# Performance work log

Measured on AMD Instinct MI355X. Metric: run time of the kernel, lower is better.

Reference implementation:

```python
import jax, jax.numpy as jnp
import numpy as np

QMAX = 127.0

def setup_inputs() -> dict:
    key = jax.random.key(0)
    k1, k2, k3 = jax.random.split(key, 3)
    x = jax.random.normal(k1, (4, 2048, 2048), dtype=jnp.float32)
    weight = jax.random.normal(k2, (2048, 2048), dtype=jnp.float32)  # [out, in]
    bias = jax.random.normal(k3, (2048,), dtype=jnp.float32)
    return {"x": x, "weight": weight, "bias": bias}

def _quantize(t):
    # per-tensor abs-max symmetric int8 quantization
    scale = jnp.max(jnp.abs(t)) / QMAX
    q = jnp.clip(jnp.round(t / scale), -128.0, 127.0).astype(jnp.int8)
    return q, scale

def reference(x, weight, bias):
    orig_shape = x.shape
    x2 = x.reshape(-1, x.shape[-1])                      # [tokens, in]
    x_q, in_scale = _quantize(x2)
    w_q, w_scale = _quantize(weight)                     # weight: [out, in]
    # int8 GEMM accumulated in int32: [tokens, out]
    acc = jnp.matmul(x_q.astype(jnp.int32), w_q.T.astype(jnp.int32))
    # dequant (output_scale = 1.0) + bias epilogue
    out = acc.astype(jnp.float32) * (in_scale * w_scale) + bias[None, :]
    return out.reshape(*orig_shape[:-1], weight.shape[0])
```

## Files before the change

kernel.cpp:

```cpp
#include <hip/hip_runtime.h>
#include <stdint.h>

#define GK 2048
#define GN 2048
#define GM 8192

#define NVX (GM * (unsigned)GK / 4)
#define NVW (GN * (unsigned)GK / 4)

#define XBLK 512
#define WBLK 128
#define QXBLK 4096
#define QWBLK 1024

typedef int i32x4 __attribute__((ext_vector_type(4)));

__device__ __forceinline__ float amax4(float4 v) {
    return fmaxf(fmaxf(fabsf(v.x), fabsf(v.y)), fmaxf(fabsf(v.z), fabsf(v.w)));
}

__global__ __launch_bounds__(256) void absmax_kernel(
    const float4* __restrict__ xv, const float4* __restrict__ wv,
    float* __restrict__ partial)
{
    const bool isx = blockIdx.x < XBLK;
    const float4* __restrict__ src = isx ? xv : wv;
    const unsigned n      = isx ? NVX : NVW;
    const unsigned b0     = isx ? blockIdx.x : blockIdx.x - XBLK;
    const unsigned stride = (isx ? XBLK : WBLK) * 256u;

    unsigned i = b0 * 256u + threadIdx.x;
    float m = 0.f;
    for (; i + 3u * stride < n; i += 4u * stride) {
        float4 a = src[i];
        float4 b = src[i + stride];
        float4 c = src[i + 2u * stride];
        float4 d = src[i + 3u * stride];
        m = fmaxf(m, fmaxf(fmaxf(amax4(a), amax4(b)),
                           fmaxf(amax4(c), amax4(d))));
    }
    for (; i < n; i += stride) m = fmaxf(m, amax4(src[i]));

    #pragma unroll
    for (int off = 32; off > 0; off >>= 1)
        m = fmaxf(m, __shfl_xor(m, off, 64));

    __shared__ float sm[4];
    const int wid = threadIdx.x >> 6;
    if ((threadIdx.x & 63) == 0) sm[wid] = m;
    __syncthreads();
    if (threadIdx.x == 0)
        partial[blockIdx.x] = fmaxf(fmaxf(sm[0], sm[1]), fmaxf(sm[2], sm[3]));
}

__global__ __launch_bounds__(256) void scale_kernel(
    const float* __restrict__ partial, float* __restrict__ scales)
{
    const int t = threadIdx.x;
    float mx = fmaxf(partial[t], partial[t + 256]);
    float mw = (t < WBLK) ? partial[XBLK + t] : 0.f;
    #pragma unroll
    for (int off = 32; off > 0; off >>= 1) {
        mx = fmaxf(mx, __shfl_xor(mx, off, 64));
        mw = fmaxf(mw, __shfl_xor(mw, off, 64));
    }
    __shared__ float smx[4], smw[4];
    const int wid = t >> 6;
    if ((t & 63) == 0) { smx[wid] = mx; smw[wid] = mw; }
    __syncthreads();
    if (t == 0) {
        float ax = fmaxf(fmaxf(smx[0], smx[1]), fmaxf(smx[2], smx[3]));
        float aw = fmaxf(fmaxf(smw[0], smw[1]), fmaxf(smw[2], smw[3]));
        float sx = ax / 127.0f;
        float sw = aw / 127.0f;
        scales[0] = sx;
        scales[1] = sw;
        scales[2] = sx * sw;
    }
}

__device__ __forceinline__ signed char quant1(float v, float s) {
    float r = rintf(v / s);
    r = fminf(fmaxf(r, -128.f), 127.f);
    return (signed char)(int)r;
}

__device__ __forceinline__ char4 quantv(float4 v, float s) {
    char4 q;
    q.x = quant1(v.x, s); q.y = quant1(v.y, s);
    q.z = quant1(v.z, s); q.w = quant1(v.w, s);
    return q;
}

__global__ __launch_bounds__(256) void quant_kernel(
    const float4* __restrict__ xv, const float4* __restrict__ wv,
    const float* __restrict__ scales,
    char4* __restrict__ xq, char4* __restrict__ wq)
{
    const bool isx = blockIdx.x < QXBLK;
    const float s = isx ? scales[0] : scales[1];
    const float4* __restrict__ src = isx ? xv : wv;
    char4* __restrict__ dst        = isx ? xq : wq;
    const unsigned b0     = isx ? blockIdx.x : blockIdx.x - QXBLK;
    const unsigned stride = (isx ? QXBLK : QWBLK) * 256u;
    const unsigned t      = b0 * 256u + threadIdx.x;

    float4 a = src[t];
    float4 b = src[t + stride];
    float4 c = src[t + 2u * stride];
    float4 d = src[t + 3u * stride];
    dst[t]               = quantv(a, s);
    dst[t + stride]      = quantv(b, s);
    dst[t + 2u * stride] = quantv(c, s);
    dst[t + 3u * stride] = quantv(d, s);
}

__global__ __launch_bounds__(256) void gemm_kernel(
    const signed char* __restrict__ Aq,
    const signed char* __restrict__ Bq,
    const float* __restrict__ bias,
    const float* __restrict__ scales,
    float* __restrict__ out)
{
    __shared__ signed char sA[128 * 128];
    __shared__ signed char sB[128 * 128];

    const int tid  = threadIdx.x;
    const int lane = tid & 63;
    const int wid  = tid >> 6;
    const int wr   = wid >> 1;
    const int wc   = wid & 1;
    const int bn   = blockIdx.x & 15;
    const int bm   = blockIdx.x >> 4;

    const int srow  = tid >> 3;
    const int sslot = tid & 7;

    i32x4 acc[4][4] = {};

    const long Abase = (long)bm * 128 * GK;
    const long Bbase = (long)bn * 128 * GK;

    for (int kt = 0; kt < GK; kt += 128) {
        #pragma unroll
        for (int j = 0; j < 4; ++j) {
            const int row  = j * 32 + srow;
            const int slot = sslot ^ (row & 7);
            const signed char* src = Aq + Abase + (long)row * GK + kt + slot * 16;
            __builtin_amdgcn_global_load_lds(
                (const __attribute__((address_space(1))) void*)src,
                (__attribute__((address_space(3))) void*)(sA + j * 4096 + wid * 1024),
                16, 0, 0);
        }
        #pragma unroll
        for (int j = 0; j < 4; ++j) {
            const int row  = j * 32 + srow;
            const int slot = sslot ^ (row & 7);
            const signed char* src = Bq + Bbase + (long)row * GK + kt + slot * 16;
            __builtin_amdgcn_global_load_lds(
                (const __attribute__((address_space(1))) void*)src,
                (__attribute__((address_space(3))) void*)(sB + j * 4096 + wid * 1024),
                16, 0, 0);
        }
        __syncthreads();

        #pragma unroll
        for (int kk = 0; kk < 2; ++kk) {
            i32x4 af[4], bf[4];
            const int g = kk * 4 + (lane >> 4);
            #pragma unroll
            for (int m = 0; m < 4; ++m) {
                const int row = wr * 64 + m * 16 + (lane & 15);
                af[m] = *(const i32x4*)(sA + row * 128 + ((g ^ (row & 7)) << 4));
            }
            #pragma unroll
            for (int n = 0; n < 4; ++n) {
                const int row = wc * 64 + n * 16 + (lane & 15);
                bf[n] = *(const i32x4*)(sB + row * 128 + ((g ^ (row & 7)) << 4));
            }
            #pragma unroll
            for (int m = 0; m < 4; ++m)
                #pragma unroll
                for (int n = 0; n < 4; ++n)
                    acc[m][n] = __builtin_amdgcn_mfma_i32_16x16x64_i8(
                        af[m], bf[n], acc[m][n], 0, 0, 0);
        }
        __syncthreads();
    }

    const float s = scales[2];
    const int orow0 = bm * 128 + wr * 64 + (lane >> 4) * 4;
    const int ocol0 = bn * 128 + wc * 64 + (lane & 15);
    #pragma unroll
    for (int n = 0; n < 4; ++n) {
        const int col = ocol0 + n * 16;
        const float bv = bias[col];
        #pragma unroll
        for (int m = 0; m < 4; ++m) {
            const int row = orow0 + m * 16;
            #pragma unroll
            for (int i = 0; i < 4; ++i) {
                out[(long)(row + i) * GN + col] = (float)acc[m][n][i] * s + bv;
            }
        }
    }
}

extern "C" void kernel_launch(void* const* d_in, const int* in_sizes, int n_in,
                              void* d_out, int out_size, void* d_ws, size_t ws_size,
                              hipStream_t stream) {
    const float* x    = (const float*)d_in[0];
    const float* w    = (const float*)d_in[1];
    const float* bias = (const float*)d_in[2];
    float* out = (float*)d_out;

    const size_t need = 4096 + (size_t)GM * GK + (size_t)GN * GK;
    if (ws_size < need) return;

    float* scales    = (float*)d_ws;
    float* partial   = (float*)d_ws + 4;
    signed char* xq  = (signed char*)d_ws + 4096;
    signed char* wq  = xq + (size_t)GM * GK;

    absmax_kernel<<<XBLK + WBLK, 256, 0, stream>>>(
        (const float4*)x, (const float4*)w, partial);
    scale_kernel<<<1, 256, 0, stream>>>(partial, scales);
    quant_kernel<<<QXBLK + QWBLK, 256, 0, stream>>>(
        (const float4*)x, (const float4*)w, scales, (char4*)xq, (char4*)wq);
    gemm_kernel<<<(GM / 128) * (GN / 128), 256, 0, stream>>>(
        xq, wq, bias, scales, out);
}
```

Baseline: 181.0 us.

## Use 32x32x32 int8 MFMA, swizzle block order, double absmax blocks

Replaces the 16x16x64 int8 MFMA tiles in the GEMM with 32x32x32 int8 MFMAs (2x2 per wave), which cuts LDS fragment loads per MFMA. It also remaps workgroup IDs so consecutive blocks are spread across the 8 XCDs, aiming at better L2 reuse of A/B tiles. The absmax reduction launches twice as many blocks for more parallelism, so the partial-buffer workspace offset grows. The epilogue is rewritten to match the 32x32 accumulator layout, with a risk of higher register pressure.

```diff
diff --git a/kernel.cpp b/kernel.cpp
--- a/kernel.cpp
+++ b/kernel.cpp
@@ -8,12 +8,13 @@
 #define NVX (GM * (unsigned)GK / 4)
 #define NVW (GN * (unsigned)GK / 4)
 
-#define XBLK 512
-#define WBLK 128
+#define XBLK 1024
+#define WBLK 256
 #define QXBLK 4096
 #define QWBLK 1024
 
-typedef int i32x4 __attribute__((ext_vector_type(4)));
+typedef int i32x4  __attribute__((ext_vector_type(4)));
+typedef int i32x16 __attribute__((ext_vector_type(16)));
 
 __device__ __forceinline__ float amax4(float4 v) {
     return fmaxf(fmaxf(fabsf(v.x), fabsf(v.y)), fmaxf(fabsf(v.z), fabsf(v.w)));
@@ -57,8 +58,9 @@
     const float* __restrict__ partial, float* __restrict__ scales)
 {
     const int t = threadIdx.x;
-    float mx = fmaxf(partial[t], partial[t + 256]);
-    float mw = (t < WBLK) ? partial[XBLK + t] : 0.f;
+    float mx = fmaxf(fmaxf(partial[t], partial[t + 256]),
+                     fmaxf(partial[t + 512], partial[t + 768]));
+    float mw = partial[XBLK + t];
     #pragma unroll
     for (int off = 32; off > 0; off >>= 1) {
         mx = fmaxf(mx, __shfl_xor(mx, off, 64));
@@ -130,13 +132,15 @@
     const int wid  = tid >> 6;
     const int wr   = wid >> 1;
     const int wc   = wid & 1;
-    const int bn   = blockIdx.x & 15;
-    const int bm   = blockIdx.x >> 4;
+
+    const int wgid = ((blockIdx.x & 7) << 7) | (blockIdx.x >> 3);
+    const int bn   = wgid & 15;
+    const int bm   = wgid >> 4;
 
     const int srow  = tid >> 3;
     const int sslot = tid & 7;
 
-    i32x4 acc[4][4] = {};
+    i32x16 acc[2][2] = {};
 
     const long Abase = (long)bm * 128 * GK;
     const long Bbase = (long)bn * 128 * GK;
@@ -165,42 +169,42 @@
         __syncthreads();
 
         #pragma unroll
-        for (int kk = 0; kk < 2; ++kk) {
-            i32x4 af[4], bf[4];
-            const int g = kk * 4 + (lane >> 4);
-            #pragma unroll
-            for (int m = 0; m < 4; ++m) {
-                const int row = wr * 64 + m * 16 + (lane & 15);
-                af[m] = *(const i32x4*)(sA + row * 128 + ((g ^ (row & 7)) << 4));
+        for (int ks = 0; ks < 4; ++ks) {
+            const int sl = ks * 2 + (lane >> 5);
+            i32x4 af[2], bf[2];
+            #pragma unroll
+            for (int m = 0; m < 2; ++m) {
+                const int row = wr * 64 + m * 32 + (lane & 31);
+                af[m] = *(const i32x4*)(sA + row * 128 + ((sl ^ (row & 7)) << 4));
             }
             #pragma unroll
-            for (int n = 0; n < 4; ++n) {
-                const int row = wc * 64 + n * 16 + (lane & 15);
-                bf[n] = *(const i32x4*)(sB + row * 128 + ((g ^ (row & 7)) << 4));
+            for (int n = 0; n < 2; ++n) {
+                const int row = wc * 64 + n * 32 + (lane & 31);
+                bf[n] = *(const i32x4*)(sB + row * 128 + ((sl ^ (row & 7)) << 4));
             }
             #pragma unroll
-            for (int m = 0; m < 4; ++m)
+            for (int m = 0; m < 2; ++m)
                 #pragma unroll
-                for (int n = 0; n < 4; ++n)
-                    acc[m][n] = __builtin_amdgcn_mfma_i32_16x16x64_i8(
+                for (int n = 0; n < 2; ++n)
+                    acc[m][n] = __builtin_amdgcn_mfma_i32_32x32x32_i8(
                         af[m], bf[n], acc[m][n], 0, 0, 0);
         }
         __syncthreads();
     }
 
     const float s = scales[2];
-    const int orow0 = bm * 128 + wr * 64 + (lane >> 4) * 4;
-    const int ocol0 = bn * 128 + wc * 64 + (lane & 15);
+    const int orow0 = bm * 128 + wr * 64 + 4 * (lane >> 5);
+    const int ocol0 = bn * 128 + wc * 64 + (lane & 31);
     #pragma unroll
-    for (int n = 0; n < 4; ++n) {
-        const int col = ocol0 + n * 16;
+    for (int n = 0; n < 2; ++n) {
+        const int col = ocol0 + n * 32;
         const float bv = bias[col];
         #pragma unroll
-        for (int m = 0; m < 4; ++m) {
-            const int row = orow0 + m * 16;
-            #pragma unroll
-            for (int i = 0; i < 4; ++i) {
-                out[(long)(row + i) * GN + col] = (float)acc[m][n][i] * s + bv;
+        for (int m = 0; m < 2; ++m) {
+            #pragma unroll
+            for (int r = 0; r < 16; ++r) {
+                const int row = orow0 + m * 32 + (r & 3) + 8 * (r >> 2);
+                out[(long)row * GN + col] = (float)acc[m][n][r] * s + bv;
             }
         }
     }
@@ -214,12 +218,12 @@
     const float* bias = (const float*)d_in[2];
     float* out = (float*)d_out;
 
-    const size_t need = 4096 + (size_t)GM * GK + (size_t)GN * GK;
+    const size_t need = 8192 + (size_t)GM * GK + (size_t)GN * GK;
     if (ws_size < need) return;
 
     float* scales    = (float*)d_ws;
     float* partial   = (float*)d_ws + 4;
-    signed char* xq  = (signed char*)d_ws + 4096;
+    signed char* xq  = (signed char*)d_ws + 8192;
     signed char* wq  = xq + (size_t)GM * GK;
 
     absmax_kernel<<<XBLK + WBLK, 256, 0, stream>>>(
```

New measurement: 181.0 us. No clear change (+0.0%).

## Double-buffer 256x256 int8 GEMM tiles and fold scale reduction into consumers

Applied to the files above, without the earlier changes.

The GEMM now uses 256x256 output tiles with 512 threads and a double-buffered 128KB LDS. The next K-tile is prefetched with global_load_lds while MFMAs run on the current one, using s_setprio and split barriers, and block IDs are remapped for better L2 locality. The separate scale kernel is removed: every quant and GEMM block re-reduces the absmax partials itself, and the partial counts are doubled. This removes one launch and hides load latency, at the cost of heavier LDS use (one block per CU), higher register pressure, and redundant per-block reductions.

```diff
diff --git a/kernel.cpp b/kernel.cpp
--- a/kernel.cpp
+++ b/kernel.cpp
@@ -8,10 +8,11 @@
 #define NVX (GM * (unsigned)GK / 4)
 #define NVW (GN * (unsigned)GK / 4)
 
-#define XBLK 512
-#define WBLK 128
+#define XBLK 1024
+#define WBLK 256
 #define QXBLK 4096
 #define QWBLK 1024
+#define NT (GK / 128)
 
 typedef int i32x4 __attribute__((ext_vector_type(4)));
 
@@ -53,30 +54,25 @@
         partial[blockIdx.x] = fmaxf(fmaxf(sm[0], sm[1]), fmaxf(sm[2], sm[3]));
 }
 
-__global__ __launch_bounds__(256) void scale_kernel(
-    const float* __restrict__ partial, float* __restrict__ scales)
-{
-    const int t = threadIdx.x;
-    float mx = fmaxf(partial[t], partial[t + 256]);
-    float mw = (t < WBLK) ? partial[XBLK + t] : 0.f;
-    #pragma unroll
-    for (int off = 32; off > 0; off >>= 1) {
-        mx = fmaxf(mx, __shfl_xor(mx, off, 64));
-        mw = fmaxf(mw, __shfl_xor(mw, off, 64));
-    }
+__device__ __forceinline__ void reduce_scales(const float* __restrict__ partial,
+                                              int tid, float* ax_out, float* aw_out)
+{
     __shared__ float smx[4], smw[4];
-    const int wid = t >> 6;
-    if ((t & 63) == 0) { smx[wid] = mx; smw[wid] = mw; }
+    float mx = 0.f, mw = 0.f;
+    if (tid < 256) {
+        mx = fmaxf(fmaxf(partial[tid], partial[tid + 256]),
+                   fmaxf(partial[tid + 512], partial[tid + 768]));
+        mw = partial[1024 + tid];
+        #pragma unroll
+        for (int off = 32; off > 0; off >>= 1) {
+            mx = fmaxf(mx, __shfl_xor(mx, off, 64));
+            mw = fmaxf(mw, __shfl_xor(mw, off, 64));
+        }
+        if ((tid & 63) == 0) { smx[tid >> 6] = mx; smw[tid >> 6] = mw; }
+    }
     __syncthreads();
-    if (t == 0) {
-        float ax = fmaxf(fmaxf(smx[0], smx[1]), fmaxf(smx[2], smx[3]));
-        float aw = fmaxf(fmaxf(smw[0], smw[1]), fmaxf(smw[2], smw[3]));
-        float sx = ax / 127.0f;
-        float sw = aw / 127.0f;
-        scales[0] = sx;
-        scales[1] = sw;
-        scales[2] = sx * sw;
-    }
+    *ax_out = fmaxf(fmaxf(smx[0], smx[1]), fmaxf(smx[2], smx[3]));
+    *aw_out = fmaxf(fmaxf(smw[0], smw[1]), fmaxf(smw[2], smw[3]));
 }
 
 __device__ __forceinline__ signed char quant1(float v, float s) {
@@ -94,11 +90,14 @@
 
 __global__ __launch_bounds__(256) void quant_kernel(
     const float4* __restrict__ xv, const float4* __restrict__ wv,
-    const float* __restrict__ scales,
+    const float* __restrict__ partial,
     char4* __restrict__ xq, char4* __restrict__ wq)
 {
+    float ax, aw;
+    reduce_scales(partial, threadIdx.x, &ax, &aw);
+
     const bool isx = blockIdx.x < QXBLK;
-    const float s = isx ? scales[0] : scales[1];
+    const float s = (isx ? ax : aw) / 127.0f;
     const float4* __restrict__ src = isx ? xv : wv;
     char4* __restrict__ dst        = isx ? xq : wq;
     const unsigned b0     = isx ? blockIdx.x : blockIdx.x - QXBLK;
@@ -115,93 +114,130 @@
     dst[t + 3u * stride] = quantv(d, s);
 }
 
-__global__ __launch_bounds__(256) void gemm_kernel(
+__global__ __launch_bounds__(512, 2) void gemm_kernel(
     const signed char* __restrict__ Aq,
     const signed char* __restrict__ Bq,
     const float* __restrict__ bias,
-    const float* __restrict__ scales,
+    const float* __restrict__ partial,
     float* __restrict__ out)
 {
-    __shared__ signed char sA[128 * 128];
-    __shared__ signed char sB[128 * 128];
+    __shared__ signed char lds[131072];
 
     const int tid  = threadIdx.x;
     const int lane = tid & 63;
     const int wid  = tid >> 6;
-    const int wr   = wid >> 1;
-    const int wc   = wid & 1;
-    const int bn   = blockIdx.x & 15;
-    const int bm   = blockIdx.x >> 4;
-
-    const int srow  = tid >> 3;
-    const int sslot = tid & 7;
-
-    i32x4 acc[4][4] = {};
-
-    const long Abase = (long)bm * 128 * GK;
-    const long Bbase = (long)bn * 128 * GK;
-
-    for (int kt = 0; kt < GK; kt += 128) {
+    const int wr   = wid >> 2;
+    const int wc   = wid & 3;
+
+    const int wgid = ((blockIdx.x & 7) << 5) | (blockIdx.x >> 3);
+    const int bn   = wgid & 7;
+    const int bm   = wgid >> 3;
+
+    float ax, aw;
+    reduce_scales(partial, tid, &ax, &aw);
+    const float s = (ax / 127.0f) * (aw / 127.0f);
+
+    const int srcslot = (tid & 7) ^ ((tid >> 3) & 7);
+    const signed char* aSrc[4]; const signed char* bSrc[4];
+    int aDst[4], bDst[4];
+    #pragma unroll
+    for (int he = 0; he < 4; ++he) {
+        const int h = he >> 1, e = he & 1;
+        const int r = h * 128 + e * 64 + (tid >> 3);
+        aSrc[he] = Aq + (long)(bm * 256 + r) * GK + srcslot * 16;
+        bSrc[he] = Bq + (long)(bn * 256 + r) * GK + srcslot * 16;
+        aDst[he] = h * 16384 + e * 8192 + tid * 16;
+        bDst[he] = 32768 + h * 16384 + e * 8192 + tid * 16;
+    }
+
+    const int lcol = lane & 15;
+    const int g0   = lane >> 4;
+    const int r7   = lcol & 7;
+    int aOff[8], bOff[4];
+    #pragma unroll
+    for (int mf = 0; mf < 8; ++mf) aOff[mf] = (wr * 128 + mf * 16 + lcol) * 128;
+    #pragma unroll
+    for (int n = 0; n < 4; ++n)    bOff[n] = 32768 + (wc * 64 + n * 16 + lcol) * 128;
+
+    i32x4 acc[8][4] = {};
+
+    #pragma unroll
+    for (int he = 0; he < 4; ++he) {
+        __builtin_amdgcn_global_load_lds(
+            (const __attribute__((address_space(1))) void*)aSrc[he],
+            (__attribute__((address_space(3))) void*)(lds + aDst[he]), 16, 0, 0);
+        __builtin_amdgcn_global_load_lds(
+            (const __attribute__((address_space(1))) void*)bSrc[he],
+            (__attribute__((address_space(3))) void*)(lds + bDst[he]), 16, 0, 0);
+    }
+    __syncthreads();
+
+    for (int t = 0; t < NT; ++t) {
+        const signed char* buf = lds + (t & 1) * 65536;
+        signed char* nbuf      = lds + ((t & 1) ^ 1) * 65536;
+        const long knext = (long)(t + 1) * 128;
+        i32x4 bf[4];
+
         #pragma unroll
-        for (int j = 0; j < 4; ++j) {
-            const int row  = j * 32 + srow;
-            const int slot = sslot ^ (row & 7);
-            const signed char* src = Aq + Abase + (long)row * GK + kt + slot * 16;
-            __builtin_amdgcn_global_load_lds(
-                (const __attribute__((address_space(1))) void*)src,
-                (__attribute__((address_space(3))) void*)(sA + j * 4096 + wid * 1024),
-                16, 0, 0);
-        }
-        #pragma unroll
-        for (int j = 0; j < 4; ++j) {
-            const int row  = j * 32 + srow;
-            const int slot = sslot ^ (row & 7);
-            const signed char* src = Bq + Bbase + (long)row * GK + kt + slot * 16;
-            __builtin_amdgcn_global_load_lds(
-                (const __attribute__((address_space(1))) void*)src,
-                (__attribute__((address_space(3))) void*)(sB + j * 4096 + wid * 1024),
-                16, 0, 0);
-        }
-        __syncthreads();
-
-        #pragma unroll
-        for (int kk = 0; kk < 2; ++kk) {
-            i32x4 af[4], bf[4];
-            const int g = kk * 4 + (lane >> 4);
-            #pragma unroll
-            for (int m = 0; m < 4; ++m) {
-                const int row = wr * 64 + m * 16 + (lane & 15);
-                af[m] = *(const i32x4*)(sA + row * 128 + ((g ^ (row & 7)) << 4));
-            }
-            #pragma unroll
-            for (int n = 0; n < 4; ++n) {
-                const int row = wc * 64 + n * 16 + (lane & 15);
-                bf[n] = *(const i32x4*)(sB + row * 128 + ((g ^ (row & 7)) << 4));
-            }
+        for (int ph = 0; ph < 4; ++ph) {
+            const int mq = ph & 1, ks = ph >> 1;
+            const int sw = ((ks * 4 + g0) ^ r7) << 4;
+
+            if ((ph & 1) == 0) {
+                #pragma unroll
+                for (int n = 0; n < 4; ++n)
+                    bf[n] = *(const i32x4*)(buf + bOff[n] + sw);
+            }
+            i32x4 af[4];
             #pragma unroll
             for (int m = 0; m < 4; ++m)
+                af[m] = *(const i32x4*)(buf + aOff[mq * 4 + m] + sw);
+
+            if (ph == 0 && t + 1 < NT) {
+                #pragma unroll
+                for (int he = 0; he < 4; ++he)
+                    __builtin_amdgcn_global_load_lds(
+                        (const __attribute__((address_space(1))) void*)(aSrc[he] + knext),
+                        (__attribute__((address_space(3))) void*)(nbuf + aDst[he]), 16, 0, 0);
+            }
+            if (ph == 1 && t + 1 < NT) {
+                #pragma unroll
+                for (int he = 0; he < 4; ++he)
+                    __builtin_amdgcn_global_load_lds(
+                        (const __attribute__((address_space(1))) void*)(bSrc[he] + knext),
+                        (__attribute__((address_space(3))) void*)(nbuf + bDst[he]), 16, 0, 0);
+            }
+
+            __builtin_amdgcn_s_barrier();
+            __builtin_amdgcn_s_setprio(1);
+            #pragma unroll
+            for (int m = 0; m < 4; ++m)
                 #pragma unroll
                 for (int n = 0; n < 4; ++n)
-                    acc[m][n] = __builtin_amdgcn_mfma_i32_16x16x64_i8(
-                        af[m], bf[n], acc[m][n], 0, 0, 0);
+                    acc[mq * 4 + m][n] = __builtin_amdgcn_mfma_i32_16x16x64_i8(
+                        af[m], bf[n], acc[mq * 4 + m][n], 0, 0, 0);
+            __builtin_amdgcn_s_setprio(0);
+
+            if (ph == 3 && t + 1 < NT) {
+                asm volatile("s_waitcnt vmcnt(0)" ::: "memory");
+                __builtin_amdgcn_sched_barrier(0);
+            }
+            __builtin_amdgcn_s_barrier();
         }
-        __syncthreads();
-    }
-
-    const float s = scales[2];
-    const int orow0 = bm * 128 + wr * 64 + (lane >> 4) * 4;
-    const int ocol0 = bn * 128 + wc * 64 + (lane & 15);
+    }
+
+    const int orow0 = bm * 256 + wr * 128 + (lane >> 4) * 4;
+    const int ocol0 = bn * 256 + wc * 64 + lcol;
     #pragma unroll
     for (int n = 0; n < 4; ++n) {
         const int col = ocol0 + n * 16;
         const float bv = bias[col];
         #pragma unroll
-        for (int m = 0; m < 4; ++m) {
-            const int row = orow0 + m * 16;
+        for (int mf = 0; mf < 8; ++mf) {
+            const int row = orow0 + mf * 16;
             #pragma unroll
-            for (int i = 0; i < 4; ++i) {
-                out[(long)(row + i) * GN + col] = (float)acc[m][n][i] * s + bv;
-            }
+            for (int i = 0; i < 4; ++i)
+                out[(long)(row + i) * GN + col] = (float)acc[mf][n][i] * s + bv;
         }
     }
 }
@@ -214,19 +250,17 @@
     const float* bias = (const float*)d_in[2];
     float* out = (float*)d_out;
 
-    const size_t need = 4096 + (size_t)GM * GK + (size_t)GN * GK;
+    const size_t need = 8192 + (size_t)GM * GK + (size_t)GN * GK;
     if (ws_size < need) return;
 
-    float* scales    = (float*)d_ws;
     float* partial   = (float*)d_ws + 4;
-    signed char* xq  = (signed char*)d_ws + 4096;
+    signed char* xq  = (signed char*)d_ws + 8192;
     signed char* wq  = xq + (size_t)GM * GK;
 
     absmax_kernel<<<XBLK + WBLK, 256, 0, stream>>>(
         (const float4*)x, (const float4*)w, partial);
-    scale_kernel<<<1, 256, 0, stream>>>(partial, scales);
     quant_kernel<<<QXBLK + QWBLK, 256, 0, stream>>>(
-        (const float4*)x, (const float4*)w, scales, (char4*)xq, (char4*)wq);
-    gemm_kernel<<<(GM / 128) * (GN / 128), 256, 0, stream>>>(
-        xq, wq, bias, scales, out);
-}
+        (const float4*)x, (const float4*)w, partial, (char4*)xq, (char4*)wq);
+    gemm_kernel<<<(GM / 256) * (GN / 256), 512, 0, stream>>>(
+        xq, wq, bias, partial, out);
+}
```

After: 175.0 us. 3.3% less time.
